# Kernel optimization log

Measured on AMD Instinct MI355X. Metric: run time of the kernel, lower is better.

## Reference

```python
import jax, jax.numpy as jnp
import numpy as np

B, S, D, H = 2, 2048, 2048, 16
HD = D // H  # head_dim = 128
ROPE_BASE = 10000.0


def _rope_tables(seq_len, head_dim, base, dtype):
    inv_freq = 1.0 / (base ** (jnp.arange(0, head_dim, 2, dtype=jnp.float32) / head_dim))
    t = jnp.arange(seq_len, dtype=jnp.float32)
    freqs = jnp.einsum('s,d->sd', t, inv_freq)           # [S, HD/2]
    emb = jnp.concatenate([freqs, freqs], axis=-1)        # [S, HD]
    return jnp.cos(emb).astype(dtype), jnp.sin(emb).astype(dtype)


def _rotate_half(x):
    half = x.shape[-1] // 2
    return jnp.concatenate([-x[..., half:], x[..., :half]], axis=-1)


def setup_inputs() -> dict:
    key = jax.random.key(0)
    kx, kq, kk, kv, ko = jax.random.split(key, 5)
    std = 0.02
    return {
        'x': jax.random.normal(kx, (B, S, D), dtype=jnp.float32),
        'Wq': jax.random.normal(kq, (D, D), dtype=jnp.float32) * std,
        'Wk': jax.random.normal(kk, (D, D), dtype=jnp.float32) * std,
        'Wv': jax.random.normal(kv, (D, D), dtype=jnp.float32) * std,
        'Wo': jax.random.normal(ko, (D, D), dtype=jnp.float32) * std,
    }


def reference(x, Wq, Wk, Wv, Wo):
    b, s, d = x.shape
    scale = HD ** -0.5
    # projections (nn.Linear: x @ W.T), split heads -> [b, h, s, hd]
    q = (x @ Wq.T).reshape(b, s, H, HD).transpose(0, 2, 1, 3)
    k = (x @ Wk.T).reshape(b, s, H, HD).transpose(0, 2, 1, 3)
    v = (x @ Wv.T).reshape(b, s, H, HD).transpose(0, 2, 1, 3)
    cos, sin = _rope_tables(s, HD, ROPE_BASE, x.dtype)    # [s, hd]
    q = q * cos + _rotate_half(q) * sin
    k = k * cos + _rotate_half(k) * sin
    scores = jnp.einsum('bhqd,bhkd->bhqk', q, k) * scale  # [b,h,s,s]
    causal = jnp.triu(jnp.ones((s, s), dtype=bool), k=1)
    scores = jnp.where(causal, jnp.float32(-jnp.inf).astype(scores.dtype), scores)
    attn = jax.nn.softmax(scores, axis=-1)
    out = jnp.einsum('bhqk,bhkd->bhqd', attn, v)
    out = out.transpose(0, 2, 1, 3).reshape(b, s, d)
    return out @ Wo.T
```

## Files before the change

kernel.cpp:

```cpp
#include <hip/hip_runtime.h>
#include <hip/hip_bf16.h>
#include <cstdint>
#include <cstddef>

#define B_ 2
#define S_ 2048
#define D_ 2048
#define H_ 16
#define HD_ 128

typedef __bf16 bf16_t;
typedef __bf16 bf16x8 __attribute__((ext_vector_type(8)));
typedef __bf16 bf16x4 __attribute__((ext_vector_type(4)));
typedef short s16x4 __attribute__((ext_vector_type(4)));
typedef float f32x4 __attribute__((ext_vector_type(4)));

__device__ __forceinline__ void async16(const bf16_t* g, bf16_t* l) {
    __builtin_amdgcn_global_load_lds(
        (const __attribute__((address_space(1))) unsigned int*)g,
        (__attribute__((address_space(3))) unsigned int*)l, 16, 0, 0);
}

__device__ __forceinline__ f32x4 mfma16x16x16_bf16(bf16x4 a, bf16x4 b, f32x4 c) {
#if __has_builtin(__builtin_amdgcn_mfma_f32_16x16x16_bf16)
    return __builtin_amdgcn_mfma_f32_16x16x16_bf16(a, b, c, 0, 0, 0);
#elif __has_builtin(__builtin_amdgcn_mfma_f32_16x16x16bf16_1k)
    return __builtin_amdgcn_mfma_f32_16x16x16bf16_1k(
        __builtin_bit_cast(s16x4, a), __builtin_bit_cast(s16x4, b), c, 0, 0, 0);
#else
    f32x4 d = c;
    asm("v_mfma_f32_16x16x16_bf16 %0, %1, %2, %0" : "+v"(d) : "v"(a), "v"(b));
    return d;
#endif
}

__global__ void f2b_multi(const float* __restrict__ x, const float* __restrict__ wq,
                          const float* __restrict__ wk, const float* __restrict__ wv,
                          const float* __restrict__ wo, bf16_t* __restrict__ xb,
                          bf16_t* __restrict__ wqb, bf16_t* __restrict__ wkb,
                          bf16_t* __restrict__ wvb, bf16_t* __restrict__ wob) {
    const float* in; bf16_t* out;
    float sc = 1.0f;
    switch (blockIdx.y) {
        case 0: in = x;            out = xb;            break;
        case 1: in = x + 4194304;  out = xb + 4194304;  break;
        case 2: in = wq;           out = wqb; sc = 0.08838834764831845f; break;
        case 3: in = wk;           out = wkb;           break;
        case 4: in = wv;           out = wvb;           break;
        default: in = wo;          out = wob;           break;
    }
    int i = (blockIdx.x * blockDim.x + threadIdx.x) * 4;
    float4 v = *(const float4*)(in + i);
    bf16x4 o = { (bf16_t)(v.x * sc), (bf16_t)(v.y * sc), (bf16_t)(v.z * sc), (bf16_t)(v.w * sc) };
    *(bf16x4*)(out + i) = o;
}


__global__ __launch_bounds__(256) void gemm_qkv(const bf16_t* __restrict__ A,
                                                const bf16_t* __restrict__ Wq,
                                                const bf16_t* __restrict__ Wk,
                                                const bf16_t* __restrict__ Wv,
                                                bf16_t* __restrict__ qb,
                                                bf16_t* __restrict__ kb,
                                                bf16_t* __restrict__ vtb) {
    __shared__ __align__(16) bf16_t sbuf[2 * 128 * 64];
    bf16_t* As = sbuf;
    bf16_t* Bs = sbuf + 8192;
    const int K = D_;
    int t = threadIdx.x;
    int w = t >> 6, lane = t & 63, lo = lane & 15, hi = lane >> 4;
    int seg = blockIdx.x >> 4;
    int n0 = (blockIdx.x & 15) * 128;
    int m0 = blockIdx.y * 128;
    const bf16_t* Bt = (seg == 0) ? Wq : (seg == 1) ? Wk : Wv;
    int wm = (w & 1) * 64, wn = (w >> 1) * 64;
    f32x4 acc[4][4] = {};
    int srow = w * 32 + (lane >> 3);
    int scol = ((lane & 7) ^ (lane >> 3)) * 8;
    const bf16_t* gA = A  + (size_t)(m0 + srow) * K + scol;
    const bf16_t* gB = Bt + (size_t)(n0 + srow) * K + scol;
    bf16_t* lA = As + w * 2048 + lane * 8;
    bf16_t* lB = Bs + w * 2048 + lane * 8;
    for (int k0 = 0; k0 < K; k0 += 64) {
#pragma unroll
        for (int i = 0; i < 4; ++i) {
            async16(gA + (size_t)(i * 8) * K + k0, lA + i * 512);
            async16(gB + (size_t)(i * 8) * K + k0, lB + i * 512);
        }
        __syncthreads();
#pragma unroll
        for (int kk = 0; kk < 2; ++kk) {
            bf16x8 af[4], bfr[4];
            int pc = (kk * 4 + hi) ^ (lo & 7);
#pragma unroll
            for (int ms = 0; ms < 4; ++ms)
                af[ms] = *(const bf16x8*)(As + (wm + ms * 16 + lo) * 64 + pc * 8);
#pragma unroll
            for (int ns = 0; ns < 4; ++ns)
                bfr[ns] = *(const bf16x8*)(Bs + (wn + ns * 16 + lo) * 64 + pc * 8);
#pragma unroll
            for (int ms = 0; ms < 4; ++ms)
#pragma unroll
                for (int ns = 0; ns < 4; ++ns)
                    acc[ms][ns] = __builtin_amdgcn_mfma_f32_16x16x32_bf16(af[ms], bfr[ns], acc[ms][ns], 0, 0, 0);
        }
        __syncthreads();
    }

    if (seg == 2) {
#pragma unroll
        for (int ms = 0; ms < 4; ++ms) {
            int mrow = m0 + wm + ms * 16 + hi * 4;
            int bb = mrow >> 11, s = mrow & (S_ - 1);
#pragma unroll
            for (int ns = 0; ns < 4; ++ns) {
                int d = n0 + wn + ns * 16 + lo;
                bf16x4 pv = { (bf16_t)acc[ms][ns][0], (bf16_t)acc[ms][ns][1],
                              (bf16_t)acc[ms][ns][2], (bf16_t)acc[ms][ns][3] };
                *(bf16x4*)(vtb + (size_t)bb * D_ * S_ + (size_t)d * S_ + s) = pv;
            }
        }
        return;
    }

    bf16_t* C = (seg == 0) ? qb : kb;
    f32x4* xt = (f32x4*)sbuf;
    int slot = w & 1;
    bool upper = (wn != 0);

    if (upper) {
#pragma unroll
        for (int ms = 0; ms < 4; ++ms)
#pragma unroll
            for (int ns = 0; ns < 4; ++ns) {
                int c = ns * 16 + lo, j = ms * 4 + hi;
                xt[slot * 1024 + c * 16 + (j ^ (c & 15))] = acc[ms][ns];
            }
    }
    __syncthreads();
    if (!upper) {
#pragma unroll
        for (int ns = 0; ns < 4; ++ns) {
            int c = ns * 16 + lo;
            float inv = __expf(-(float)c * 0.14391156831212787f);
#pragma unroll
            for (int ms = 0; ms < 4; ++ms) {
                int j = ms * 4 + hi;
                f32x4 pv = xt[slot * 1024 + c * 16 + (j ^ (c & 15))];
#pragma unroll
                for (int r = 0; r < 4; ++r) {
                    int row = m0 + wm + ms * 16 + hi * 4 + r;
                    float ang = (float)(row & (S_ - 1)) * inv;
                    float sn, cs;
                    __sincosf(ang, &sn, &cs);
                    C[(size_t)row * D_ + n0 + c] = (bf16_t)(acc[ms][ns][r] * cs - pv[r] * sn);
                }
            }
        }
    }
    __syncthreads();
    if (!upper) {
#pragma unroll
        for (int ms = 0; ms < 4; ++ms)
#pragma unroll
            for (int ns = 0; ns < 4; ++ns) {
                int c = ns * 16 + lo, j = ms * 4 + hi;
                xt[slot * 1024 + c * 16 + (j ^ (c & 15))] = acc[ms][ns];
            }
    }
    __syncthreads();
    if (upper) {
#pragma unroll
        for (int ns = 0; ns < 4; ++ns) {
            int c = ns * 16 + lo;
            float inv = __expf(-(float)c * 0.14391156831212787f);
#pragma unroll
            for (int ms = 0; ms < 4; ++ms) {
                int j = ms * 4 + hi;
                f32x4 pv = xt[slot * 1024 + c * 16 + (j ^ (c & 15))];
#pragma unroll
                for (int r = 0; r < 4; ++r) {
                    int row = m0 + wm + ms * 16 + hi * 4 + r;
                    float ang = (float)(row & (S_ - 1)) * inv;
                    float sn, cs;
                    __sincosf(ang, &sn, &cs);
                    C[(size_t)row * D_ + n0 + 64 + c] = (bf16_t)(acc[ms][ns][r] * cs + pv[r] * sn);
                }
            }
        }
    }
}

__global__ __launch_bounds__(256) void gemm_bt_f32(const bf16_t* __restrict__ A,
                                                   const bf16_t* __restrict__ Bt,
                                                   float* __restrict__ C,
                                                   int M, int N, int K) {
    __shared__ __align__(16) bf16_t As[128 * 64];
    __shared__ __align__(16) bf16_t Bs[128 * 64];
    int t = threadIdx.x;
    int w = t >> 6, lane = t & 63, lo = lane & 15, hi = lane >> 4;
    int m0 = blockIdx.y * 128, n0 = blockIdx.x * 128;
    int wm = (w & 1) * 64, wn = (w >> 1) * 64;
    f32x4 acc[4][4] = {};
    int srow = w * 32 + (lane >> 3);
    int scol = ((lane & 7) ^ (lane >> 3)) * 8;
    const bf16_t* gA = A  + (size_t)(m0 + srow) * K + scol;
    const bf16_t* gB = Bt + (size_t)(n0 + srow) * K + scol;
    bf16_t* lA = As + w * 2048 + lane * 8;
    bf16_t* lB = Bs + w * 2048 + lane * 8;
    for (int k0 = 0; k0 < K; k0 += 64) {
#pragma unroll
        for (int i = 0; i < 4; ++i) {
            async16(gA + (size_t)(i * 8) * K + k0, lA + i * 512);
            async16(gB + (size_t)(i * 8) * K + k0, lB + i * 512);
        }
        __syncthreads();
#pragma unroll
        for (int kk = 0; kk < 2; ++kk) {
            bf16x8 af[4], bfr[4];
            int pc = (kk * 4 + hi) ^ (lo & 7);
#pragma unroll
            for (int ms = 0; ms < 4; ++ms)
                af[ms] = *(const bf16x8*)(As + (wm + ms * 16 + lo) * 64 + pc * 8);
#pragma unroll
            for (int ns = 0; ns < 4; ++ns)
                bfr[ns] = *(const bf16x8*)(Bs + (wn + ns * 16 + lo) * 64 + pc * 8);
#pragma unroll
            for (int ms = 0; ms < 4; ++ms)
#pragma unroll
                for (int ns = 0; ns < 4; ++ns)
                    acc[ms][ns] = __builtin_amdgcn_mfma_f32_16x16x32_bf16(af[ms], bfr[ns], acc[ms][ns], 0, 0, 0);
        }
        __syncthreads();
    }
#pragma unroll
    for (int ms = 0; ms < 4; ++ms)
#pragma unroll
        for (int ns = 0; ns < 4; ++ns)
#pragma unroll
            for (int r = 0; r < 4; ++r)
                C[(size_t)(m0 + wm + ms * 16 + hi * 4 + r) * N + n0 + wn + ns * 16 + lo] = acc[ms][ns][r];
}

__global__ __launch_bounds__(512) void attn_kernel(const bf16_t* __restrict__ q,
                                                   const bf16_t* __restrict__ k,
                                                   const bf16_t* __restrict__ vt,
                                                   bf16_t* __restrict__ o) {
    __shared__ __align__(16) bf16_t Ks[2][128 * 128];
    __shared__ __align__(16) bf16_t Vs[2][128 * 128];
    int t = threadIdx.x;
    int w = t >> 6, lane = t & 63, lo = lane & 15, hi = lane >> 4;
    int bx = blockIdx.x;
    int b = blockIdx.y >> 4, h = blockIdx.y & 15;
    const size_t head_off = (size_t)b * S_ * D_ + (size_t)h * HD_;
    const size_t vhead_off = ((size_t)b * D_ + (size_t)h * HD_) * S_;

#pragma unroll 1
    for (int pass = 0; pass < 2; ++pass) {
        int qt = pass ? (15 - bx) : bx;
        int q0 = qt * 128;
        int qg = q0 + w * 16 + lo;
        bf16x8 aq[4];
#pragma unroll
        for (int c = 0; c < 4; ++c)
            aq[c] = *(const bf16x8*)(q + head_off + (size_t)qg * D_ + c * 32 + hi * 8);

        float l_part = 0.f;
        f32x4 oacc[8] = {};
        int nkt = qt + 1;

        {
#pragma unroll
            for (int i = 0; i < 4; ++i) {
                int chunk = w * 4 + i;
                int r = chunk * 4 + hi;
                async16(k + head_off + (size_t)r * D_ + (lo ^ (r & 15)) * 8,
                        Ks[0] + chunk * 512 + lane * 8);
            }
#pragma unroll
            for (int i = 0; i < 4; ++i) {
                int chunk = w * 4 + i;
                int d = chunk * 4 + hi;
                async16(vt + vhead_off + (size_t)d * S_ + (lo ^ (d & 15)) * 8,
                        Vs[0] + chunk * 512 + lane * 8);
            }
        }
        __syncthreads();

        for (int kt = 0; kt < nkt; ++kt) {
            int k0 = kt * 128;
            int cb = kt & 1;
            if (kt + 1 < nkt) {
                int kn = k0 + 128;
#pragma unroll
                for (int i = 0; i < 4; ++i) {
                    int chunk = w * 4 + i;
                    int r = chunk * 4 + hi;
                    async16(k + head_off + (size_t)(kn + r) * D_ + (lo ^ (r & 15)) * 8,
                            Ks[cb ^ 1] + chunk * 512 + lane * 8);
                }
#pragma unroll
                for (int i = 0; i < 4; ++i) {
                    int chunk = w * 4 + i;
                    int d = chunk * 4 + hi;
                    async16(vt + vhead_off + (size_t)d * S_ + kn + (lo ^ (d & 15)) * 8,
                            Vs[cb ^ 1] + chunk * 512 + lane * 8);
                }
            }

            const bf16_t* Kb = Ks[cb];
            const bf16_t* Vb = Vs[cb];
            f32x4 sacc[8] = {};
#pragma unroll
            for (int c = 0; c < 4; ++c) {
#pragma unroll
                for (int nt = 0; nt < 8; ++nt) {
                    int row = nt * 16 + lo;
                    int pc = (c * 4 + hi) ^ lo;
                    bf16x8 ak = *(const bf16x8*)(Kb + row * 128 + pc * 8);
                    sacc[nt] = __builtin_amdgcn_mfma_f32_16x16x32_bf16(ak, aq[c], sacc[nt], 0, 0, 0);
                }
            }
            bool diag = (kt == qt);
            bf16x4 pf[8];
#pragma unroll
            for (int nt = 0; nt < 8; ++nt) {
#pragma unroll
                for (int r = 0; r < 4; ++r) {
                    float e = __expf(fminf(sacc[nt][r], 60.f));
                    if (diag) {
                        int kg = k0 + nt * 16 + hi * 4 + r;
                        if (kg > qg) e = 0.f;
                    }
                    l_part += e;
                    pf[nt][r] = (bf16_t)e;
                }
            }
#pragma unroll
            for (int nt = 0; nt < 8; ++nt) {
                int kkb = nt * 16 + hi * 4;
                int c16 = kkb >> 3, rem = kkb & 7;
#pragma unroll
                for (int dt = 0; dt < 8; ++dt) {
                    int d = dt * 16 + lo;
                    bf16x4 av = *(const bf16x4*)(Vb + d * 128 + (c16 ^ (d & 15)) * 8 + rem);
                    oacc[dt] = mfma16x16x16_bf16(av, pf[nt], oacc[dt]);
                }
            }
            __syncthreads();
        }
        float l = l_part;
        l += __shfl_xor(l, 16);
        l += __shfl_xor(l, 32);
        float rl = 1.0f / l;
#pragma unroll
        for (int dt = 0; dt < 8; ++dt) {
            bf16x4 ov = { (bf16_t)(oacc[dt][0] * rl), (bf16_t)(oacc[dt][1] * rl),
                          (bf16_t)(oacc[dt][2] * rl), (bf16_t)(oacc[dt][3] * rl) };
            *(bf16x4*)(o + head_off + (size_t)qg * D_ + dt * 16 + hi * 4) = ov;
        }
    }
}

extern "C" void kernel_launch(void* const* d_in, const int* in_sizes, int n_in,
                              void* d_out, int out_size, void* d_ws, size_t ws_size,
                              hipStream_t stream) {
    (void)in_sizes; (void)n_in; (void)out_size; (void)ws_size;
    const float* x  = (const float*)d_in[0];
    const float* Wq = (const float*)d_in[1];
    const float* Wk = (const float*)d_in[2];
    const float* Wv = (const float*)d_in[3];
    const float* Wo = (const float*)d_in[4];
    char* ws = (char*)d_ws;
    bf16_t* xb  = (bf16_t*)(ws);
    bf16_t* Wqb = (bf16_t*)(ws + 16777216);
    bf16_t* Wkb = (bf16_t*)(ws + 25165824);
    bf16_t* Wvb = (bf16_t*)(ws + 33554432);
    bf16_t* Wob = (bf16_t*)(ws + 41943040);
    bf16_t* qb  = (bf16_t*)(ws + 50331648);
    bf16_t* kb  = (bf16_t*)(ws + 67108864);
    bf16_t* vtb = (bf16_t*)(ws + 83886080);
    bf16_t* ob  = (bf16_t*)(ws + 100663296);
    float* out = (float*)d_out;

    f2b_multi<<<dim3(4096, 6), 256, 0, stream>>>(x, Wq, Wk, Wv, Wo, xb, Wqb, Wkb, Wvb, Wob);

    gemm_qkv<<<dim3(48, 32), 256, 0, stream>>>(xb, Wqb, Wkb, Wvb, qb, kb, vtb);

    attn_kernel<<<dim3(8, B_ * H_), 512, 0, stream>>>(qb, kb, vtb, ob);

    gemm_bt_f32<<<dim3(D_ / 128, (B_ * S_) / 128), 256, 0, stream>>>(ob, Wob, out, B_ * S_, D_, D_);
}
```

Before: 371.8 us.

## Split attention key tile across two wave groups with shared-memory output reduction

Each wave now handles 32 query rows instead of 16, and the 8 waves split into two groups that each process half of the 128-key tile. Every K and V fragment read from LDS therefore feeds two MFMAs, which halves LDS read traffic per unit of compute. Partial outputs and row sums are combined through shared memory at the end of each pass, which costs extra syncs and LDS stores. Launch bounds also request 2 blocks per CU, which may force register spilling given the doubled accumulators.

```diff
diff --git a/kernel.cpp b/kernel.cpp
--- a/kernel.cpp
+++ b/kernel.cpp
@@ -242,14 +242,17 @@
                 C[(size_t)(m0 + wm + ms * 16 + hi * 4 + r) * N + n0 + wn + ns * 16 + lo] = acc[ms][ns][r];
 }
 
-__global__ __launch_bounds__(512) void attn_kernel(const bf16_t* __restrict__ q,
-                                                   const bf16_t* __restrict__ k,
-                                                   const bf16_t* __restrict__ vt,
-                                                   bf16_t* __restrict__ o) {
+__global__ __launch_bounds__(512, 2) void attn_kernel(const bf16_t* __restrict__ q,
+                                                      const bf16_t* __restrict__ k,
+                                                      const bf16_t* __restrict__ vt,
+                                                      bf16_t* __restrict__ o) {
     __shared__ __align__(16) bf16_t Ks[2][128 * 128];
     __shared__ __align__(16) bf16_t Vs[2][128 * 128];
+    __shared__ float lred[4][2][16];
     int t = threadIdx.x;
     int w = t >> 6, lane = t & 63, lo = lane & 15, hi = lane >> 4;
+    int kh = w >> 2;
+    int wq = w & 3;
     int bx = blockIdx.x;
     int b = blockIdx.y >> 4, h = blockIdx.y & 15;
     const size_t head_off = (size_t)b * S_ * D_ + (size_t)h * HD_;
@@ -259,31 +262,32 @@
     for (int pass = 0; pass < 2; ++pass) {
         int qt = pass ? (15 - bx) : bx;
         int q0 = qt * 128;
-        int qg = q0 + w * 16 + lo;
-        bf16x8 aq[4];
-#pragma unroll
-        for (int c = 0; c < 4; ++c)
-            aq[c] = *(const bf16x8*)(q + head_off + (size_t)qg * D_ + c * 32 + hi * 8);
-
-        float l_part = 0.f;
-        f32x4 oacc[8] = {};
+        int qg0 = q0 + wq * 32 + lo;
+        int qg1 = qg0 + 16;
+        bf16x8 aq[2][4];
+#pragma unroll
+        for (int c = 0; c < 4; ++c) {
+            aq[0][c] = *(const bf16x8*)(q + head_off + (size_t)qg0 * D_ + c * 32 + hi * 8);
+            aq[1][c] = *(const bf16x8*)(q + head_off + (size_t)qg1 * D_ + c * 32 + hi * 8);
+        }
+
+        float l0 = 0.f, l1 = 0.f;
+        f32x4 oacc[8][2] = {};
         int nkt = qt + 1;
 
-        {
-#pragma unroll
-            for (int i = 0; i < 4; ++i) {
-                int chunk = w * 4 + i;
-                int r = chunk * 4 + hi;
-                async16(k + head_off + (size_t)r * D_ + (lo ^ (r & 15)) * 8,
-                        Ks[0] + chunk * 512 + lane * 8);
-            }
-#pragma unroll
-            for (int i = 0; i < 4; ++i) {
-                int chunk = w * 4 + i;
-                int d = chunk * 4 + hi;
-                async16(vt + vhead_off + (size_t)d * S_ + (lo ^ (d & 15)) * 8,
-                        Vs[0] + chunk * 512 + lane * 8);
-            }
+#pragma unroll
+        for (int i = 0; i < 4; ++i) {
+            int chunk = w * 4 + i;
+            int r = chunk * 4 + hi;
+            async16(k + head_off + (size_t)r * D_ + (lo ^ (r & 15)) * 8,
+                    Ks[0] + chunk * 512 + lane * 8);
+        }
+#pragma unroll
+        for (int i = 0; i < 4; ++i) {
+            int chunk = w * 4 + i;
+            int d = chunk * 4 + hi;
+            async16(vt + vhead_off + (size_t)d * S_ + (lo ^ (d & 15)) * 8,
+                    Vs[0] + chunk * 512 + lane * 8);
         }
         __syncthreads();
 
@@ -310,55 +314,81 @@
 
             const bf16_t* Kb = Ks[cb];
             const bf16_t* Vb = Vs[cb];
-            f32x4 sacc[8] = {};
+            f32x4 sacc[4][2] = {};
 #pragma unroll
             for (int c = 0; c < 4; ++c) {
 #pragma unroll
-                for (int nt = 0; nt < 8; ++nt) {
-                    int row = nt * 16 + lo;
+                for (int nt = 0; nt < 4; ++nt) {
+                    int row = kh * 64 + nt * 16 + lo;
                     int pc = (c * 4 + hi) ^ lo;
                     bf16x8 ak = *(const bf16x8*)(Kb + row * 128 + pc * 8);
-                    sacc[nt] = __builtin_amdgcn_mfma_f32_16x16x32_bf16(ak, aq[c], sacc[nt], 0, 0, 0);
+                    sacc[nt][0] = __builtin_amdgcn_mfma_f32_16x16x32_bf16(ak, aq[0][c], sacc[nt][0], 0, 0, 0);
+                    sacc[nt][1] = __builtin_amdgcn_mfma_f32_16x16x32_bf16(ak, aq[1][c], sacc[nt][1], 0, 0, 0);
                 }
             }
             bool diag = (kt == qt);
-            bf16x4 pf[8];
-#pragma unroll
-            for (int nt = 0; nt < 8; ++nt) {
+            bf16x4 pf[4][2];
+#pragma unroll
+            for (int nt = 0; nt < 4; ++nt) {
 #pragma unroll
                 for (int r = 0; r < 4; ++r) {
-                    float e = __expf(fminf(sacc[nt][r], 60.f));
+                    int kg = k0 + kh * 64 + nt * 16 + hi * 4 + r;
+                    float e0 = __expf(fminf(sacc[nt][0][r], 60.f));
+                    float e1 = __expf(fminf(sacc[nt][1][r], 60.f));
                     if (diag) {
-                        int kg = k0 + nt * 16 + hi * 4 + r;
-                        if (kg > qg) e = 0.f;
+                        if (kg > qg0) e0 = 0.f;
+                        if (kg > qg1) e1 = 0.f;
                     }
-                    l_part += e;
-                    pf[nt][r] = (bf16_t)e;
-                }
-            }
-#pragma unroll
-            for (int nt = 0; nt < 8; ++nt) {
-                int kkb = nt * 16 + hi * 4;
+                    l0 += e0; l1 += e1;
+                    pf[nt][0][r] = (bf16_t)e0;
+                    pf[nt][1][r] = (bf16_t)e1;
+                }
+            }
+#pragma unroll
+            for (int nt = 0; nt < 4; ++nt) {
+                int kkb = kh * 64 + nt * 16 + hi * 4;
                 int c16 = kkb >> 3, rem = kkb & 7;
 #pragma unroll
                 for (int dt = 0; dt < 8; ++dt) {
                     int d = dt * 16 + lo;
                     bf16x4 av = *(const bf16x4*)(Vb + d * 128 + (c16 ^ (d & 15)) * 8 + rem);
-                    oacc[dt] = mfma16x16x16_bf16(av, pf[nt], oacc[dt]);
+                    oacc[dt][0] = mfma16x16x16_bf16(av, pf[nt][0], oacc[dt][0]);
+                    oacc[dt][1] = mfma16x16x16_bf16(av, pf[nt][1], oacc[dt][1]);
                 }
             }
             __syncthreads();
         }
-        float l = l_part;
-        l += __shfl_xor(l, 16);
-        l += __shfl_xor(l, 32);
-        float rl = 1.0f / l;
-#pragma unroll
-        for (int dt = 0; dt < 8; ++dt) {
-            bf16x4 ov = { (bf16_t)(oacc[dt][0] * rl), (bf16_t)(oacc[dt][1] * rl),
-                          (bf16_t)(oacc[dt][2] * rl), (bf16_t)(oacc[dt][3] * rl) };
-            *(bf16x4*)(o + head_off + (size_t)qg * D_ + dt * 16 + hi * 4) = ov;
-        }
+
+        l0 += __shfl_xor(l0, 16); l0 += __shfl_xor(l0, 32);
+        l1 += __shfl_xor(l1, 16); l1 += __shfl_xor(l1, 32);
+        f32x4* red = (f32x4*)Ks;
+        if (w >= 4) {
+            f32x4* rp = red + (size_t)(w - 4) * 1024;
+#pragma unroll
+            for (int dt = 0; dt < 8; ++dt) {
+                rp[(dt * 2 + 0) * 64 + lane] = oacc[dt][0];
+                rp[(dt * 2 + 1) * 64 + lane] = oacc[dt][1];
+            }
+            if (hi == 0) { lred[w - 4][0][lo] = l0; lred[w - 4][1][lo] = l1; }
+        }
+        __syncthreads();
+        if (w < 4) {
+            f32x4* rp = red + (size_t)w * 1024;
+            float rl0 = 1.0f / (l0 + lred[w][0][lo]);
+            float rl1 = 1.0f / (l1 + lred[w][1][lo]);
+#pragma unroll
+            for (int dt = 0; dt < 8; ++dt) {
+                f32x4 p0 = rp[(dt * 2 + 0) * 64 + lane];
+                f32x4 p1 = rp[(dt * 2 + 1) * 64 + lane];
+                bf16x4 o0 = { (bf16_t)((oacc[dt][0][0] + p0[0]) * rl0), (bf16_t)((oacc[dt][0][1] + p0[1]) * rl0),
+                              (bf16_t)((oacc[dt][0][2] + p0[2]) * rl0), (bf16_t)((oacc[dt][0][3] + p0[3]) * rl0) };
+                bf16x4 o1 = { (bf16_t)((oacc[dt][1][0] + p1[0]) * rl1), (bf16_t)((oacc[dt][1][1] + p1[1]) * rl1),
+                              (bf16_t)((oacc[dt][1][2] + p1[2]) * rl1), (bf16_t)((oacc[dt][1][3] + p1[3]) * rl1) };
+                *(bf16x4*)(o + head_off + (size_t)qg0 * D_ + dt * 16 + hi * 4) = o0;
+                *(bf16x4*)(o + head_off + (size_t)qg1 * D_ + dt * 16 + hi * 4) = o1;
+            }
+        }
+        __syncthreads();
     }
 }
 
```

Measured after the change: 360.2 us. -3.1%, faster.
